# Optimization experiments

Measured on AMD Instinct MI355X. Metric: run time of the kernel, lower is better.

The kernel has to match this reference:

```python
import jax, jax.numpy as jnp
import numpy as np

HIDDEN = 1024
D_MEM = 256
BATCH = 4
SEQ = 1024
EPS = 1e-6


def elu_plus_one(x):
    # F.elu(x) + 1 == exp(x) for x<0, x+1 for x>=0 (positive feature map)
    return jnp.where(x > 0, x + 1.0, jnp.exp(x))


def setup_inputs() -> dict:
    key = jax.random.key(0)
    ks = jax.random.split(key, 8)
    hidden_states = jax.random.normal(ks[0], (BATCH, SEQ, HIDDEN), dtype=jnp.float32)
    s = 1.0 / np.sqrt(HIDDEN)
    w_q = jax.random.normal(ks[1], (D_MEM, HIDDEN), dtype=jnp.float32) * s
    w_k = jax.random.normal(ks[2], (D_MEM, HIDDEN), dtype=jnp.float32) * s
    w_v = jax.random.normal(ks[3], (D_MEM, HIDDEN), dtype=jnp.float32) * s
    w_o = jax.random.normal(ks[4], (HIDDEN, D_MEM), dtype=jnp.float32) * (1.0 / np.sqrt(D_MEM))
    gate = jnp.zeros((1,), dtype=jnp.float32)
    # nonzero persistent memory state so retrieval path is exercised
    memory = jax.random.normal(ks[5], (D_MEM, D_MEM), dtype=jnp.float32) * 0.1
    memory_norm = jax.random.uniform(ks[6], (D_MEM,), dtype=jnp.float32) * 10.0 + 1.0
    return {
        "hidden_states": hidden_states,
        "w_q": w_q, "w_k": w_k, "w_v": w_v, "w_o": w_o,
        "gate": gate, "memory": memory, "memory_norm": memory_norm,
    }


def _retrieve(sigma_x, memory, memory_norm):
    # [b,s,d] @ [d,d] -> [b,s,d], normalized by sigma_x @ memory_norm
    a_unnorm = jnp.matmul(sigma_x, memory)
    norm = jnp.clip(jnp.matmul(sigma_x, memory_norm), EPS, None)[..., None]
    out = a_unnorm / norm
    # torch: if memory_norm.sum() < 1e-6 -> zeros
    return jnp.where(memory_norm.sum() < EPS, jnp.zeros_like(out), out)


def reference(hidden_states, w_q, w_k, w_v, w_o, gate, memory, memory_norm):
    b, s, _ = hidden_states.shape
    q = jnp.einsum('bsh,dh->bsd', hidden_states, w_q)
    k = jnp.einsum('bsh,dh->bsd', hidden_states, w_k)
    v = jnp.einsum('bsh,dh->bsd', hidden_states, w_v)

    sigma_q = elu_plus_one(q)
    sigma_k = elu_plus_one(k)

    # --- retrieval from compressive memory ---
    memory_output = _retrieve(sigma_q, memory, memory_norm)

    # --- causal linear attention within segment (cumsum form, as in source) ---
    kv = jnp.einsum('bsd,bse->bsde', sigma_k, v)          # [b,s,d,d]
    kv_cumsum = jnp.cumsum(kv, axis=1)                     # [b,s,d,d]
    k_cumsum = jnp.cumsum(sigma_k, axis=1)                 # [b,s,d]
    numerator = jnp.einsum('bsd,bsde->bse', sigma_q, kv_cumsum)
    denominator = jnp.clip(jnp.einsum('bsd,bsd->bs', sigma_q, k_cumsum), EPS, None)[..., None]
    local_output = numerator / denominator

    g = jax.nn.sigmoid(gate[0])
    combined = g * memory_output + (1.0 - g) * local_output
    output = jnp.einsum('bsd,hd->bsh', combined, w_o)

    # --- delta-rule memory update (detached in torch) ---
    retrieved_unnorm = jnp.matmul(sigma_k, memory)
    norm = jnp.clip(jnp.matmul(sigma_k, memory_norm), EPS, None)[..., None]
    delta_v = v - retrieved_unnorm / norm
    memory_update = jnp.einsum('bsd,bse->de', sigma_k, delta_v) / (b * s)
    new_memory = jax.lax.stop_gradient(memory + memory_update)
    z_update = sigma_k.sum(axis=(0, 1)) / b
    new_memory_norm = jax.lax.stop_gradient(memory_norm + z_update)

    return output, new_memory, new_memory_norm
```

## Files before the change

### kernel.cpp

```cpp
#include <hip/hip_runtime.h>


#define HIDDEN 1024
#define DMEM 256
#define BATCH 4
#define SEQ 1024
#define MTOT (BATCH * SEQ)
#define CHUNK 128
#define NCH (SEQ / CHUNK)
#define NCHT (BATCH * NCH)
#define EPSF 1e-6f

typedef __bf16 bf16x8 __attribute__((ext_vector_type(8)));
typedef __bf16 bf16x4 __attribute__((ext_vector_type(4)));
typedef float f32x4 __attribute__((ext_vector_type(4)));

#define GL_LDS(g, l)                                                                   \
  __builtin_amdgcn_global_load_lds((const __attribute__((address_space(1))) void*)(g), \
                                   (__attribute__((address_space(3))) void*)(l), 16, 0, 0)

__device__ __forceinline__ float elu1(float x) { return x > 0.f ? x + 1.f : __expf(x); }

__device__ __forceinline__ void stage128(const __bf16* p, long ld, int k0, __bf16* sm,
                                         int wave) {
  GL_LDS(p + k0, sm + wave * 512);
  GL_LDS(p + (size_t)64 * ld + k0, sm + 2048 + wave * 512);
  GL_LDS(p + k0 + 32, sm + 4096 + wave * 512);
  GL_LDS(p + (size_t)64 * ld + k0 + 32, sm + 4096 + 2048 + wave * 512);
}
__device__ __forceinline__ void stage64(const __bf16* p, int k0, __bf16* sm, int wave) {
  GL_LDS(p + k0, sm + wave * 512);
  GL_LDS(p + k0 + 32, sm + 2048 + wave * 512);
}

__device__ __forceinline__ void gemm128_bk64(const __bf16* aptr, long lda, const __bf16* bptr,
                                             long ldb, int klen, __bf16* smA, __bf16* smB,
                                             int wave, int wr, int wc, int quad, int l16,
                                             f32x4 (&acc)[4][4]) {
  for (int k0 = 0; k0 < klen; k0 += 64) {
    stage128(aptr, lda, k0, smA, wave);
    stage128(bptr, ldb, k0, smB, wave);
    __syncthreads();
#pragma unroll
    for (int h = 0; h < 2; ++h) {
      bf16x8 aF[4], bF[4];
#pragma unroll
      for (int i = 0; i < 4; ++i)
        aF[i] = *reinterpret_cast<const bf16x8*>(smA + h * 4096 +
                                                 (wr * 64 + i * 16 + l16) * 32 + quad * 8);
#pragma unroll
      for (int j = 0; j < 4; ++j)
        bF[j] = *reinterpret_cast<const bf16x8*>(smB + h * 4096 +
                                                 (wc * 64 + j * 16 + l16) * 32 + quad * 8);
#pragma unroll
      for (int i = 0; i < 4; ++i)
#pragma unroll
        for (int j = 0; j < 4; ++j)
          acc[i][j] = __builtin_amdgcn_mfma_f32_16x16x32_bf16(aF[i], bF[j], acc[i][j], 0, 0, 0);
    }
    __syncthreads();
  }
}

__device__ __forceinline__ void gemm64_bk64(const __bf16* aptr, const __bf16* bptr, long ldb,
                                            int klen, __bf16* smA, __bf16* smB, int wave,
                                            int wr, int wc, int quad, int l16,
                                            f32x4 (&acc)[2][4]) {
  for (int k0 = 0; k0 < klen; k0 += 64) {
    stage64(aptr, k0, smA, wave);
    stage128(bptr, ldb, k0, smB, wave);
    __syncthreads();
#pragma unroll
    for (int h = 0; h < 2; ++h) {
      bf16x8 aF[2], bF[4];
#pragma unroll
      for (int i = 0; i < 2; ++i)
        aF[i] = *reinterpret_cast<const bf16x8*>(smA + h * 2048 +
                                                 (wr * 32 + i * 16 + l16) * 32 + quad * 8);
#pragma unroll
      for (int j = 0; j < 4; ++j)
        bF[j] = *reinterpret_cast<const bf16x8*>(smB + h * 4096 +
                                                 (wc * 64 + j * 16 + l16) * 32 + quad * 8);
#pragma unroll
      for (int i = 0; i < 2; ++i)
#pragma unroll
        for (int j = 0; j < 4; ++j)
          acc[i][j] = __builtin_amdgcn_mfma_f32_16x16x32_bf16(aF[i], bF[j], acc[i][j], 0, 0, 0);
    }
    __syncthreads();
  }
}

__global__ void kprep(const float* __restrict__ hs, const float* __restrict__ wq,
                      const float* __restrict__ wk, const float* __restrict__ wv,
                      const float* __restrict__ wo, const float* __restrict__ mem,
                      __bf16* __restrict__ hsb, __bf16* __restrict__ wqkvb,
                      __bf16* __restrict__ wob, __bf16* __restrict__ memT,
                      float* __restrict__ out) {
  __shared__ float s[64][65];
  int b = blockIdx.x, tid = threadIdx.x;
  if (b < 4096) {
    int i = b * 256 + tid;
    float4 f = reinterpret_cast<const float4*>(hs)[i];
    bf16x4 h = {(__bf16)f.x, (__bf16)f.y, (__bf16)f.z, (__bf16)f.w};
    reinterpret_cast<bf16x4*>(hsb)[i] = h;
  } else if (b < 5120) {
    int y = (b - 4096) >> 8;
    const float* src = (y == 0) ? wq : (y == 1) ? wk : (y == 2) ? wv : wo;
    __bf16* dst = (y < 3) ? wqkvb + (size_t)y * (DMEM * HIDDEN) : wob;
    int i = ((b - 4096) & 255) * 256 + tid;
    float4 f = reinterpret_cast<const float4*>(src)[i];
    bf16x4 h = {(__bf16)f.x, (__bf16)f.y, (__bf16)f.z, (__bf16)f.w};
    reinterpret_cast<bf16x4*>(dst)[i] = h;
  } else if (b < 5136) {
    int t = b - 5120;
    int bx = t & 3, by = t >> 2;
    int r0 = tid >> 6, col = tid & 63;
#pragma unroll
    for (int it = 0; it < 16; ++it) {
      int row = it * 4 + r0;
      s[row][col] = mem[(size_t)(by * 64 + row) * DMEM + bx * 64 + col];
    }
    __syncthreads();
#pragma unroll
    for (int it = 0; it < 16; ++it) {
      int row = it * 4 + r0;
      memT[(size_t)(bx * 64 + row) * DMEM + by * 64 + col] = (__bf16)s[col][row];
    }
  } else {
    int g = (b - 5136) * 256 + tid;
    reinterpret_cast<float4*>(out + (size_t)MTOT * HIDDEN)[g] =
        reinterpret_cast<const float4*>(mem)[g];
  }
}

__global__ __launch_bounds__(256) void k1_qkv_mfma(
    const __bf16* __restrict__ X, const __bf16* __restrict__ W, __bf16* __restrict__ sqb,
    __bf16* __restrict__ skb, __bf16* __restrict__ skT, __bf16* __restrict__ vT) {
  __shared__ __bf16 As[4096];
  __shared__ __bf16 Bs[8192];
  int tid = threadIdx.x;
  int lane = tid & 63, wave = tid >> 6;
  int m0 = blockIdx.x * 64;
  int by = blockIdx.y;
  int wsel = by >> 1, n0 = (by & 1) * 128;
  const __bf16* aptr = X + (size_t)(m0 + (tid >> 2)) * HIDDEN + ((tid & 3) << 3);
  const __bf16* bptr = W + (size_t)(by * 128 + (tid >> 2)) * HIDDEN + ((tid & 3) << 3);
  int wr = wave >> 1, wc = wave & 1, quad = lane >> 4, l16 = lane & 15;
  f32x4 acc[2][4] = {};
  gemm64_bk64(aptr, bptr, HIDDEN, HIDDEN, As, Bs, wave, wr, wc, quad, l16, acc);
#pragma unroll
  for (int i = 0; i < 2; ++i)
#pragma unroll
    for (int j = 0; j < 4; ++j) {
      int mb = m0 + wr * 32 + i * 16 + quad * 4;
      int n = n0 + wc * 64 + j * 16 + l16;
      if (wsel == 0) {
#pragma unroll
        for (int r = 0; r < 4; ++r) sqb[(size_t)(mb + r) * DMEM + n] = (__bf16)elu1(acc[i][j][r]);
      } else if (wsel == 1) {
        bf16x4 t;
#pragma unroll
        for (int r = 0; r < 4; ++r) {
          float v = elu1(acc[i][j][r]);
          skb[(size_t)(mb + r) * DMEM + n] = (__bf16)v;
          t[r] = (__bf16)v;
        }
        *reinterpret_cast<bf16x4*>(skT + (size_t)n * MTOT + mb) = t;
      } else {
        bf16x4 t;
#pragma unroll
        for (int r = 0; r < 4; ++r) t[r] = (__bf16)acc[i][j][r];
        *reinterpret_cast<bf16x4*>(vT + (size_t)n * MTOT + mb) = t;
      }
    }
}

__global__ __launch_bounds__(256) void kC(const __bf16* __restrict__ vT,
                                          const __bf16* __restrict__ skT,
                                          const __bf16* __restrict__ sqb,
                                          const __bf16* __restrict__ skb,
                                          __bf16* __restrict__ kvcT, __bf16* __restrict__ scb,
                                          float* __restrict__ ksc) {
  __shared__ __bf16 As[4096];
  __shared__ __bf16 Bs[8192];
  int tid = threadIdx.x;
  int c = blockIdx.x;
  int y = blockIdx.y;
  if (y == 10) {
    int d = tid;
    float s = 0.f;
    for (int i = 0; i < CHUNK; ++i) s += (float)skb[(size_t)(c * CHUNK + i) * DMEM + d];
    ksc[c * DMEM + d] = s;
    return;
  }
  int lane = tid & 63, wave = tid >> 6;
  int wr = wave >> 1, wc = wave & 1, quad = lane >> 4, l16 = lane & 15;
  if (y < 8) {
    int e0 = (y >> 1) * 64, d0 = (y & 1) * 128;
    const __bf16* aptr = vT + (size_t)(e0 + (tid >> 2)) * MTOT + c * CHUNK + ((tid & 3) << 3);
    const __bf16* bptr = skT + (size_t)(d0 + (tid >> 2)) * MTOT + c * CHUNK + ((tid & 3) << 3);
    f32x4 acc[2][4] = {};
    gemm64_bk64(aptr, bptr, MTOT, CHUNK, As, Bs, wave, wr, wc, quad, l16, acc);
#pragma unroll
    for (int i = 0; i < 2; ++i)
#pragma unroll
      for (int j = 0; j < 4; ++j)
#pragma unroll
        for (int r = 0; r < 4; ++r) {
          int e = e0 + wr * 32 + i * 16 + quad * 4 + r;
          int d = d0 + wc * 64 + j * 16 + l16;
          kvcT[(size_t)c * DMEM * DMEM + (size_t)e * DMEM + d] = (__bf16)acc[i][j][r];
        }
  } else {
    int i0 = (y - 8) * 64;
    const __bf16* aptr = sqb + (size_t)(c * CHUNK + i0 + (tid >> 2)) * DMEM + ((tid & 3) << 3);
    const __bf16* bptr = skb + (size_t)(c * CHUNK + (tid >> 2)) * DMEM + ((tid & 3) << 3);
    f32x4 acc[2][4] = {};
    gemm64_bk64(aptr, bptr, DMEM, DMEM, As, Bs, wave, wr, wc, quad, l16, acc);
#pragma unroll
    for (int i = 0; i < 2; ++i)
#pragma unroll
      for (int j = 0; j < 4; ++j)
#pragma unroll
        for (int r = 0; r < 4; ++r) {
          int ii = i0 + wr * 32 + i * 16 + quad * 4 + r;
          int jj = wc * 64 + j * 16 + l16;
          scb[(size_t)c * CHUNK * CHUNK + (size_t)ii * CHUNK + jj] =
              (jj <= ii) ? (__bf16)acc[i][j][r] : (__bf16)0.f;
        }
  }
}

__global__ __launch_bounds__(256) void kD(const __bf16* __restrict__ kvcT,
                                          __bf16* __restrict__ kvpT,
                                          const float* __restrict__ ksc,
                                          const __bf16* __restrict__ scb,
                                          const __bf16* __restrict__ sqb,
                                          const __bf16* __restrict__ skb,
                                          const float* __restrict__ mnorm,
                                          float* __restrict__ den, float* __restrict__ qn,
                                          float* __restrict__ kn) {
  int vt = blockIdx.x;
  int tid = threadIdx.x;
  if (vt < 128) {
    int batch = vt >> 5;
    size_t idx8 = (size_t)(((vt & 31) * 256 + tid)) * 8;
    bf16x8 t[NCH];
#pragma unroll
    for (int c = 0; c < NCH; ++c)
      t[c] = *reinterpret_cast<const bf16x8*>(kvcT +
                                              (size_t)(batch * NCH + c) * DMEM * DMEM + idx8);
    float run[8] = {};
#pragma unroll
    for (int c = 0; c < NCH; ++c) {
      bf16x8 o;
#pragma unroll
      for (int r = 0; r < 8; ++r) o[r] = (__bf16)run[r];
      *reinterpret_cast<bf16x8*>(kvpT + (size_t)(batch * NCH + c) * DMEM * DMEM + idx8) = o;
#pragma unroll
      for (int r = 0; r < 8; ++r) run[r] += (float)t[c][r];
    }
  } else {
    int wave = tid >> 6, lane = tid & 63;
    int m = (vt - 128) * 4 + wave;
    int c = m >> 7;
    int i = m & 127;
    int cb = c & ~7;
    int cnt = c - cb;
    float s_sc = 0.f, s_d2 = 0.f, s_qn = 0.f, s_kn = 0.f;
    for (int j = lane; j < CHUNK; j += 64)
      s_sc += (float)scb[(size_t)c * CHUNK * CHUNK + (size_t)i * CHUNK + j];
    for (int d = lane; d < DMEM; d += 64) {
      float q = (float)sqb[(size_t)m * DMEM + d];
      float k = (float)skb[(size_t)m * DMEM + d];
      float kp = 0.f;
#pragma unroll
      for (int cc = 0; cc < 7; ++cc) {
        float v = ksc[(cb + cc) * DMEM + d];
        kp += (cc < cnt) ? v : 0.f;
      }
      s_d2 += q * kp;
      s_qn += q * mnorm[d];
      s_kn += k * mnorm[d];
    }
#pragma unroll
    for (int off = 32; off > 0; off >>= 1) {
      s_sc += __shfl_down(s_sc, off);
      s_d2 += __shfl_down(s_d2, off);
      s_qn += __shfl_down(s_qn, off);
      s_kn += __shfl_down(s_kn, off);
    }
    if (lane == 0) {
      den[m] = s_sc + s_d2;
      qn[m] = s_qn;
      kn[m] = s_kn;
    }
  }
}

__global__ __launch_bounds__(256) void kE(const __bf16* __restrict__ scb,
                                          const __bf16* __restrict__ sqb,
                                          const __bf16* __restrict__ skb,
                                          const __bf16* __restrict__ vT,
                                          const __bf16* __restrict__ kvpT,
                                          const __bf16* __restrict__ memT,
                                          const float* __restrict__ den,
                                          const float* __restrict__ qn,
                                          const float* __restrict__ kn,
                                          const float* __restrict__ gate,
                                          const float* __restrict__ mnorm,
                                          __bf16* __restrict__ combb, __bf16* __restrict__ dvT) {
  __shared__ __bf16 As[4096];
  __shared__ __bf16 B1s[8192];
  __shared__ __bf16 B2s[8192];
  __shared__ float warr[4];
  int tid = threadIdx.x;
  int lane = tid & 63, wave = tid >> 6;
  int wr = wave >> 1, wc = wave & 1, quad = lane >> 4, l16 = lane & 15;
  int bid = blockIdx.x;
  if (bid < 128) {
    float mv = mnorm[tid];
#pragma unroll
    for (int off = 32; off > 0; off >>= 1) mv += __shfl_down(mv, off);
    if (lane == 0) warr[wave] = mv;
    __syncthreads();
    float fl = ((warr[0] + warr[1] + warr[2] + warr[3]) < EPSF) ? 0.f : 1.f;
    __syncthreads();
    int c = bid >> 2, yy = bid & 3;
    int i0 = (yy >> 1) * 64, e0 = (yy & 1) * 128;
    f32x4 acc_loc[2][4] = {};
    f32x4 acc_mem[2][4] = {};
    {
      const __bf16* aptr =
          scb + (size_t)c * CHUNK * CHUNK + (size_t)(i0 + (tid >> 2)) * CHUNK + ((tid & 3) << 3);
      const __bf16* bptr = vT + (size_t)(e0 + (tid >> 2)) * MTOT + c * CHUNK + ((tid & 3) << 3);
      gemm64_bk64(aptr, bptr, MTOT, CHUNK, As, B1s, wave, wr, wc, quad, l16, acc_loc);
    }
    {
      const __bf16* aptr = sqb + (size_t)(c * CHUNK + i0 + (tid >> 2)) * DMEM + ((tid & 3) << 3);
      const __bf16* b1ptr =
          kvpT + (size_t)c * DMEM * DMEM + (size_t)(e0 + (tid >> 2)) * DMEM + ((tid & 3) << 3);
      const __bf16* b2ptr = memT + (size_t)(e0 + (tid >> 2)) * DMEM + ((tid & 3) << 3);
      for (int k0 = 0; k0 < DMEM; k0 += 64) {
        stage64(aptr, k0, As, wave);
        stage128(b1ptr, DMEM, k0, B1s, wave);
        stage128(b2ptr, DMEM, k0, B2s, wave);
        __syncthreads();
#pragma unroll
        for (int h = 0; h < 2; ++h) {
          bf16x8 aF[2], b1F[4], b2F[4];
#pragma unroll
          for (int i = 0; i < 2; ++i)
            aF[i] = *reinterpret_cast<const bf16x8*>(As + h * 2048 +
                                                     (wr * 32 + i * 16 + l16) * 32 + quad * 8);
#pragma unroll
          for (int j = 0; j < 4; ++j) {
            b1F[j] = *reinterpret_cast<const bf16x8*>(B1s + h * 4096 +
                                                      (wc * 64 + j * 16 + l16) * 32 + quad * 8);
            b2F[j] = *reinterpret_cast<const bf16x8*>(B2s + h * 4096 +
                                                      (wc * 64 + j * 16 + l16) * 32 + quad * 8);
          }
#pragma unroll
          for (int i = 0; i < 2; ++i)
#pragma unroll
            for (int j = 0; j < 4; ++j) {
              acc_loc[i][j] =
                  __builtin_amdgcn_mfma_f32_16x16x32_bf16(aF[i], b1F[j], acc_loc[i][j], 0, 0, 0);
              acc_mem[i][j] =
                  __builtin_amdgcn_mfma_f32_16x16x32_bf16(aF[i], b2F[j], acc_mem[i][j], 0, 0, 0);
            }
        }
        __syncthreads();
      }
    }
    float g = 1.f / (1.f + __expf(-gate[0]));
#pragma unroll
    for (int i = 0; i < 2; ++i) {
      int mb = c * CHUNK + i0 + wr * 32 + i * 16 + quad * 4;
      float dn[4], qv[4];
#pragma unroll
      for (int r = 0; r < 4; ++r) {
        dn[r] = fmaxf(den[mb + r], EPSF);
        qv[r] = fmaxf(qn[mb + r], EPSF);
      }
#pragma unroll
      for (int j = 0; j < 4; ++j) {
        int e = e0 + wc * 64 + j * 16 + l16;
#pragma unroll
        for (int r = 0; r < 4; ++r) {
          float comb = g * fl * acc_mem[i][j][r] / qv[r] + (1.f - g) * acc_loc[i][j][r] / dn[r];
          combb[(size_t)(mb + r) * DMEM + e] = (__bf16)comb;
        }
      }
    }
  } else {
    int t = bid - 128;
    int m0 = (t >> 1) * 64, n0 = (t & 1) * 128;
    const __bf16* aptr = skb + (size_t)(m0 + (tid >> 2)) * DMEM + ((tid & 3) << 3);
    const __bf16* bptr = memT + (size_t)(n0 + (tid >> 2)) * DMEM + ((tid & 3) << 3);
    f32x4 acc[2][4] = {};
    gemm64_bk64(aptr, bptr, DMEM, DMEM, As, B1s, wave, wr, wc, quad, l16, acc);
#pragma unroll
    for (int i = 0; i < 2; ++i) {
      int mb = m0 + wr * 32 + i * 16 + quad * 4;
      float kv[4];
#pragma unroll
      for (int r = 0; r < 4; ++r) kv[r] = fmaxf(kn[mb + r], EPSF);
#pragma unroll
      for (int j = 0; j < 4; ++j) {
        int n = n0 + wc * 64 + j * 16 + l16;
        bf16x4 vv = *reinterpret_cast<const bf16x4*>(vT + (size_t)n * MTOT + mb);
        bf16x4 tt;
#pragma unroll
        for (int r = 0; r < 4; ++r) tt[r] = (__bf16)((float)vv[r] - acc[i][j][r] / kv[r]);
        *reinterpret_cast<bf16x4*>(dvT + (size_t)n * MTOT + mb) = tt;
      }
    }
  }
}

__global__ __launch_bounds__(256) void kF(const __bf16* __restrict__ combb,
                                          const __bf16* __restrict__ wob,
                                          const __bf16* __restrict__ skT,
                                          const __bf16* __restrict__ dvT,
                                          const float* __restrict__ ksc,
                                          const float* __restrict__ mnorm,
                                          float* __restrict__ out) {
  __shared__ __bf16 As[8192];
  __shared__ __bf16 Bs[8192];
  int tid = threadIdx.x;
  int bid = blockIdx.x;
  if (bid == 384) {
    int d = tid;
    float s = 0.f;
    for (int c = 0; c < NCHT; ++c) s += ksc[c * DMEM + d];
    out[(size_t)MTOT * HIDDEN + DMEM * DMEM + d] = mnorm[d] + s * (1.f / (float)BATCH);
    return;
  }
  int lane = tid & 63, wave = tid >> 6;
  int wr = wave >> 1, wc = wave & 1, quad = lane >> 4, l16 = lane & 15;
  if (bid < 256) {
    int m0 = (bid & 31) * 128, by = bid >> 5;
    const __bf16* aptr = combb + (size_t)(m0 + (tid >> 2)) * DMEM + ((tid & 3) << 3);
    const __bf16* bptr = wob + (size_t)(by * 128 + (tid >> 2)) * DMEM + ((tid & 3) << 3);
    f32x4 acc[4][4] = {};
    gemm128_bk64(aptr, DMEM, bptr, DMEM, DMEM, As, Bs, wave, wr, wc, quad, l16, acc);
#pragma unroll
    for (int i = 0; i < 4; ++i)
#pragma unroll
      for (int j = 0; j < 4; ++j)
#pragma unroll
        for (int r = 0; r < 4; ++r) {
          int m = m0 + wr * 64 + i * 16 + quad * 4 + r;
          int n = by * 128 + wc * 64 + j * 16 + l16;
          out[(size_t)m * HIDDEN + n] = acc[i][j][r];
        }
  } else {
    int t = bid - 256;
    int kbase = (t >> 3) * 256;
    int yy = t & 7;
    int d0 = (yy >> 1) * 64, e0 = (yy & 1) * 128;
    const __bf16* aptr = skT + (size_t)(d0 + (tid >> 2)) * MTOT + kbase + ((tid & 3) << 3);
    const __bf16* bptr = dvT + (size_t)(e0 + (tid >> 2)) * MTOT + kbase + ((tid & 3) << 3);
    f32x4 acc[2][4] = {};
    gemm64_bk64(aptr, bptr, MTOT, 256, As, Bs, wave, wr, wc, quad, l16, acc);
    float* base = out + (size_t)MTOT * HIDDEN;
#pragma unroll
    for (int i = 0; i < 2; ++i)
#pragma unroll
      for (int j = 0; j < 4; ++j)
#pragma unroll
        for (int r = 0; r < 4; ++r) {
          int d = d0 + wr * 32 + i * 16 + quad * 4 + r;
          int e = e0 + wc * 64 + j * 16 + l16;
          atomicAdd(&base[(size_t)d * DMEM + e], acc[i][j][r] * (1.f / (float)MTOT));
        }
  }
}

extern "C" void kernel_launch(void* const* d_in, const int* in_sizes, int n_in,
                              void* d_out, int out_size, void* d_ws, size_t ws_size,
                              hipStream_t stream) {
  const float* hs = (const float*)d_in[0];
  const float* wq = (const float*)d_in[1];
  const float* wk = (const float*)d_in[2];
  const float* wv = (const float*)d_in[3];
  const float* wo = (const float*)d_in[4];
  const float* gate = (const float*)d_in[5];
  const float* mem = (const float*)d_in[6];
  const float* mnorm = (const float*)d_in[7];
  float* out = (float*)d_out;
  float* ws = (float*)d_ws;

  float* ksc = ws;
  float* den = ksc + 8192;
  float* qn = den + 4096;
  float* kn = qn + 4096;
  __bf16* kvcT = (__bf16*)(ws + 20480);
  __bf16* hsb = kvcT + (size_t)NCHT * DMEM * DMEM;
  __bf16* wqkvb = hsb + (size_t)MTOT * HIDDEN;
  __bf16* wob = wqkvb + (size_t)3 * DMEM * HIDDEN;
  __bf16* memT = wob + (size_t)HIDDEN * DMEM;
  __bf16* sqb = memT + (size_t)DMEM * DMEM;
  __bf16* skb = sqb + (size_t)MTOT * DMEM;
  __bf16* skT = skb + (size_t)MTOT * DMEM;
  __bf16* vT = skT + (size_t)MTOT * DMEM;
  __bf16* scb = vT + (size_t)MTOT * DMEM;
  __bf16* kvpT = scb + (size_t)NCHT * CHUNK * CHUNK;
  __bf16* combb = kvpT + (size_t)NCHT * DMEM * DMEM;
  __bf16* dvT = combb + (size_t)MTOT * DMEM;

  kprep<<<dim3(5200), 256, 0, stream>>>(hs, wq, wk, wv, wo, mem, hsb, wqkvb, wob, memT, out);
  k1_qkv_mfma<<<dim3(64, 6), 256, 0, stream>>>(hsb, wqkvb, sqb, skb, skT, vT);
  kC<<<dim3(NCHT, 11), 256, 0, stream>>>(vT, skT, sqb, skb, kvcT, scb, ksc);
  kD<<<dim3(1152), 256, 0, stream>>>(kvcT, kvpT, ksc, scb, sqb, skb, mnorm, den, qn, kn);
  kE<<<dim3(256), 256, 0, stream>>>(scb, sqb, skb, vT, kvpT, memT, den, qn, kn, gate, mnorm,
                                    combb, dvT);
  kF<<<dim3(385), 256, 0, stream>>>(combb, wob, skT, dvT, ksc, mnorm, out);
}
```

Measured before the change: 135.0 us.

## Rebalance grids: smaller QKV/out tiles, move delta-v computation into kC

The QKV projection kernel moves from 64x128 to 64x64 tiles, doubling its grid to 768 blocks. The out-projection in kF moves from 128x128 to 64x128 tiles, giving 512 blocks. The delta-v computation (sigma_k @ memory, normalised, subtracted from v) moves from kE into extra blocks of kC, which now computes its own k-norm dot product, so kE runs only the combine path. The aim is more parallelism on a GPU with many CUs and less load imbalance in kE, in exchange for less data reuse per tile.

```diff
diff --git a/kernel.cpp b/kernel.cpp
--- a/kernel.cpp
+++ b/kernel.cpp
@@ -33,35 +33,6 @@
   GL_LDS(p + k0 + 32, sm + 2048 + wave * 512);
 }
 
-__device__ __forceinline__ void gemm128_bk64(const __bf16* aptr, long lda, const __bf16* bptr,
-                                             long ldb, int klen, __bf16* smA, __bf16* smB,
-                                             int wave, int wr, int wc, int quad, int l16,
-                                             f32x4 (&acc)[4][4]) {
-  for (int k0 = 0; k0 < klen; k0 += 64) {
-    stage128(aptr, lda, k0, smA, wave);
-    stage128(bptr, ldb, k0, smB, wave);
-    __syncthreads();
-#pragma unroll
-    for (int h = 0; h < 2; ++h) {
-      bf16x8 aF[4], bF[4];
-#pragma unroll
-      for (int i = 0; i < 4; ++i)
-        aF[i] = *reinterpret_cast<const bf16x8*>(smA + h * 4096 +
-                                                 (wr * 64 + i * 16 + l16) * 32 + quad * 8);
-#pragma unroll
-      for (int j = 0; j < 4; ++j)
-        bF[j] = *reinterpret_cast<const bf16x8*>(smB + h * 4096 +
-                                                 (wc * 64 + j * 16 + l16) * 32 + quad * 8);
-#pragma unroll
-      for (int i = 0; i < 4; ++i)
-#pragma unroll
-        for (int j = 0; j < 4; ++j)
-          acc[i][j] = __builtin_amdgcn_mfma_f32_16x16x32_bf16(aF[i], bF[j], acc[i][j], 0, 0, 0);
-    }
-    __syncthreads();
-  }
-}
-
 __device__ __forceinline__ void gemm64_bk64(const __bf16* aptr, const __bf16* bptr, long ldb,
                                             int klen, __bf16* smA, __bf16* smB, int wave,
                                             int wr, int wc, int quad, int l16,
@@ -85,6 +56,35 @@
       for (int i = 0; i < 2; ++i)
 #pragma unroll
         for (int j = 0; j < 4; ++j)
+          acc[i][j] = __builtin_amdgcn_mfma_f32_16x16x32_bf16(aF[i], bF[j], acc[i][j], 0, 0, 0);
+    }
+    __syncthreads();
+  }
+}
+
+__device__ __forceinline__ void gemm64x64_bk64(const __bf16* aptr, const __bf16* bptr,
+                                               int klen, __bf16* smA, __bf16* smB, int wave,
+                                               int wr, int wc, int quad, int l16,
+                                               f32x4 (&acc)[2][2]) {
+  for (int k0 = 0; k0 < klen; k0 += 64) {
+    stage64(aptr, k0, smA, wave);
+    stage64(bptr, k0, smB, wave);
+    __syncthreads();
+#pragma unroll
+    for (int h = 0; h < 2; ++h) {
+      bf16x8 aF[2], bF[2];
+#pragma unroll
+      for (int i = 0; i < 2; ++i)
+        aF[i] = *reinterpret_cast<const bf16x8*>(smA + h * 2048 +
+                                                 (wr * 32 + i * 16 + l16) * 32 + quad * 8);
+#pragma unroll
+      for (int j = 0; j < 2; ++j)
+        bF[j] = *reinterpret_cast<const bf16x8*>(smB + h * 2048 +
+                                                 (wc * 32 + j * 16 + l16) * 32 + quad * 8);
+#pragma unroll
+      for (int i = 0; i < 2; ++i)
+#pragma unroll
+        for (int j = 0; j < 2; ++j)
           acc[i][j] = __builtin_amdgcn_mfma_f32_16x16x32_bf16(aF[i], bF[j], acc[i][j], 0, 0, 0);
     }
     __syncthreads();
@@ -138,23 +138,24 @@
     const __bf16* __restrict__ X, const __bf16* __restrict__ W, __bf16* __restrict__ sqb,
     __bf16* __restrict__ skb, __bf16* __restrict__ skT, __bf16* __restrict__ vT) {
   __shared__ __bf16 As[4096];
-  __shared__ __bf16 Bs[8192];
+  __shared__ __bf16 Bs[4096];
   int tid = threadIdx.x;
   int lane = tid & 63, wave = tid >> 6;
   int m0 = blockIdx.x * 64;
   int by = blockIdx.y;
-  int wsel = by >> 1, n0 = (by & 1) * 128;
+  int wsel = by >> 2, n0 = (by & 3) * 64;
   const __bf16* aptr = X + (size_t)(m0 + (tid >> 2)) * HIDDEN + ((tid & 3) << 3);
-  const __bf16* bptr = W + (size_t)(by * 128 + (tid >> 2)) * HIDDEN + ((tid & 3) << 3);
+  const __bf16* bptr =
+      W + (size_t)(wsel * DMEM + n0 + (tid >> 2)) * HIDDEN + ((tid & 3) << 3);
   int wr = wave >> 1, wc = wave & 1, quad = lane >> 4, l16 = lane & 15;
-  f32x4 acc[2][4] = {};
-  gemm64_bk64(aptr, bptr, HIDDEN, HIDDEN, As, Bs, wave, wr, wc, quad, l16, acc);
+  f32x4 acc[2][2] = {};
+  gemm64x64_bk64(aptr, bptr, HIDDEN, As, Bs, wave, wr, wc, quad, l16, acc);
 #pragma unroll
   for (int i = 0; i < 2; ++i)
 #pragma unroll
-    for (int j = 0; j < 4; ++j) {
+    for (int j = 0; j < 2; ++j) {
       int mb = m0 + wr * 32 + i * 16 + quad * 4;
-      int n = n0 + wc * 64 + j * 16 + l16;
+      int n = n0 + wc * 32 + j * 16 + l16;
       if (wsel == 0) {
 #pragma unroll
         for (int r = 0; r < 4; ++r) sqb[(size_t)(mb + r) * DMEM + n] = (__bf16)elu1(acc[i][j][r]);
@@ -176,14 +177,17 @@
     }
 }
 
-__global__ __launch_bounds__(256) void kC(const __bf16* __restrict__ vT,
-                                          const __bf16* __restrict__ skT,
-                                          const __bf16* __restrict__ sqb,
-                                          const __bf16* __restrict__ skb,
-                                          __bf16* __restrict__ kvcT, __bf16* __restrict__ scb,
-                                          float* __restrict__ ksc) {
+__global__ __launch_bounds__(256) void kC2(const __bf16* __restrict__ vT,
+                                           const __bf16* __restrict__ skT,
+                                           const __bf16* __restrict__ sqb,
+                                           const __bf16* __restrict__ skb,
+                                           const __bf16* __restrict__ memT,
+                                           const float* __restrict__ mnorm,
+                                           __bf16* __restrict__ kvcT, __bf16* __restrict__ scb,
+                                           float* __restrict__ ksc, __bf16* __restrict__ dvT) {
   __shared__ __bf16 As[4096];
   __shared__ __bf16 Bs[8192];
+  __shared__ float knl[64];
   int tid = threadIdx.x;
   int c = blockIdx.x;
   int y = blockIdx.y;
@@ -212,7 +216,7 @@
           int d = d0 + wc * 64 + j * 16 + l16;
           kvcT[(size_t)c * DMEM * DMEM + (size_t)e * DMEM + d] = (__bf16)acc[i][j][r];
         }
-  } else {
+  } else if (y < 10) {
     int i0 = (y - 8) * 64;
     const __bf16* aptr = sqb + (size_t)(c * CHUNK + i0 + (tid >> 2)) * DMEM + ((tid & 3) << 3);
     const __bf16* bptr = skb + (size_t)(c * CHUNK + (tid >> 2)) * DMEM + ((tid & 3) << 3);
@@ -229,6 +233,38 @@
           scb[(size_t)c * CHUNK * CHUNK + (size_t)ii * CHUNK + jj] =
               (jj <= ii) ? (__bf16)acc[i][j][r] : (__bf16)0.f;
         }
+  } else {
+    int t = (y - 11) * 32 + c;
+    int m0 = (t >> 1) * 64, n0 = (t & 1) * 128;
+    for (int rr = 0; rr < 16; ++rr) {
+      int m = m0 + wave * 16 + rr;
+      float s = 0.f;
+      for (int d = lane; d < DMEM; d += 64) s += (float)skb[(size_t)m * DMEM + d] * mnorm[d];
+#pragma unroll
+      for (int off = 32; off > 0; off >>= 1) s += __shfl_down(s, off);
+      if (lane == 0) knl[wave * 16 + rr] = s;
+    }
+    __syncthreads();
+    const __bf16* aptr = skb + (size_t)(m0 + (tid >> 2)) * DMEM + ((tid & 3) << 3);
+    const __bf16* bptr = memT + (size_t)(n0 + (tid >> 2)) * DMEM + ((tid & 3) << 3);
+    f32x4 acc[2][4] = {};
+    gemm64_bk64(aptr, bptr, DMEM, DMEM, As, Bs, wave, wr, wc, quad, l16, acc);
+#pragma unroll
+    for (int i = 0; i < 2; ++i) {
+      int rel = wr * 32 + i * 16 + quad * 4;
+      float kv[4];
+#pragma unroll
+      for (int r = 0; r < 4; ++r) kv[r] = fmaxf(knl[rel + r], EPSF);
+#pragma unroll
+      for (int j = 0; j < 4; ++j) {
+        int n = n0 + wc * 64 + j * 16 + l16;
+        bf16x4 vv = *reinterpret_cast<const bf16x4*>(vT + (size_t)n * MTOT + m0 + rel);
+        bf16x4 tt;
+#pragma unroll
+        for (int r = 0; r < 4; ++r) tt[r] = (__bf16)((float)vv[r] - acc[i][j][r] / kv[r]);
+        *reinterpret_cast<bf16x4*>(dvT + (size_t)n * MTOT + m0 + rel) = tt;
+      }
+    }
   }
 }
 
@@ -237,10 +273,8 @@
                                           const float* __restrict__ ksc,
                                           const __bf16* __restrict__ scb,
                                           const __bf16* __restrict__ sqb,
-                                          const __bf16* __restrict__ skb,
                                           const float* __restrict__ mnorm,
-                                          float* __restrict__ den, float* __restrict__ qn,
-                                          float* __restrict__ kn) {
+                                          float* __restrict__ den, float* __restrict__ qn) {
   int vt = blockIdx.x;
   int tid = threadIdx.x;
   if (vt < 128) {
@@ -268,12 +302,11 @@
     int i = m & 127;
     int cb = c & ~7;
     int cnt = c - cb;
-    float s_sc = 0.f, s_d2 = 0.f, s_qn = 0.f, s_kn = 0.f;
+    float s_sc = 0.f, s_d2 = 0.f, s_qn = 0.f;
     for (int j = lane; j < CHUNK; j += 64)
       s_sc += (float)scb[(size_t)c * CHUNK * CHUNK + (size_t)i * CHUNK + j];
     for (int d = lane; d < DMEM; d += 64) {
       float q = (float)sqb[(size_t)m * DMEM + d];
-      float k = (float)skb[(size_t)m * DMEM + d];
       float kp = 0.f;
 #pragma unroll
       for (int cc = 0; cc < 7; ++cc) {
@@ -282,35 +315,30 @@
       }
       s_d2 += q * kp;
       s_qn += q * mnorm[d];
-      s_kn += k * mnorm[d];
     }
 #pragma unroll
     for (int off = 32; off > 0; off >>= 1) {
       s_sc += __shfl_down(s_sc, off);
       s_d2 += __shfl_down(s_d2, off);
       s_qn += __shfl_down(s_qn, off);
-      s_kn += __shfl_down(s_kn, off);
     }
     if (lane == 0) {
       den[m] = s_sc + s_d2;
       qn[m] = s_qn;
-      kn[m] = s_kn;
     }
   }
 }
 
 __global__ __launch_bounds__(256) void kE(const __bf16* __restrict__ scb,
                                           const __bf16* __restrict__ sqb,
-                                          const __bf16* __restrict__ skb,
                                           const __bf16* __restrict__ vT,
                                           const __bf16* __restrict__ kvpT,
                                           const __bf16* __restrict__ memT,
                                           const float* __restrict__ den,
                                           const float* __restrict__ qn,
-                                          const float* __restrict__ kn,
                                           const float* __restrict__ gate,
                                           const float* __restrict__ mnorm,
-                                          __bf16* __restrict__ combb, __bf16* __restrict__ dvT) {
+                                          __bf16* __restrict__ combb) {
   __shared__ __bf16 As[4096];
   __shared__ __bf16 B1s[8192];
   __shared__ __bf16 B2s[8192];
@@ -319,102 +347,77 @@
   int lane = tid & 63, wave = tid >> 6;
   int wr = wave >> 1, wc = wave & 1, quad = lane >> 4, l16 = lane & 15;
   int bid = blockIdx.x;
-  if (bid < 128) {
-    float mv = mnorm[tid];
-#pragma unroll
-    for (int off = 32; off > 0; off >>= 1) mv += __shfl_down(mv, off);
-    if (lane == 0) warr[wave] = mv;
-    __syncthreads();
-    float fl = ((warr[0] + warr[1] + warr[2] + warr[3]) < EPSF) ? 0.f : 1.f;
-    __syncthreads();
-    int c = bid >> 2, yy = bid & 3;
-    int i0 = (yy >> 1) * 64, e0 = (yy & 1) * 128;
-    f32x4 acc_loc[2][4] = {};
-    f32x4 acc_mem[2][4] = {};
-    {
-      const __bf16* aptr =
-          scb + (size_t)c * CHUNK * CHUNK + (size_t)(i0 + (tid >> 2)) * CHUNK + ((tid & 3) << 3);
-      const __bf16* bptr = vT + (size_t)(e0 + (tid >> 2)) * MTOT + c * CHUNK + ((tid & 3) << 3);
-      gemm64_bk64(aptr, bptr, MTOT, CHUNK, As, B1s, wave, wr, wc, quad, l16, acc_loc);
-    }
-    {
-      const __bf16* aptr = sqb + (size_t)(c * CHUNK + i0 + (tid >> 2)) * DMEM + ((tid & 3) << 3);
-      const __bf16* b1ptr =
-          kvpT + (size_t)c * DMEM * DMEM + (size_t)(e0 + (tid >> 2)) * DMEM + ((tid & 3) << 3);
-      const __bf16* b2ptr = memT + (size_t)(e0 + (tid >> 2)) * DMEM + ((tid & 3) << 3);
-      for (int k0 = 0; k0 < DMEM; k0 += 64) {
-        stage64(aptr, k0, As, wave);
-        stage128(b1ptr, DMEM, k0, B1s, wave);
-        stage128(b2ptr, DMEM, k0, B2s, wave);
-        __syncthreads();
-#pragma unroll
-        for (int h = 0; h < 2; ++h) {
-          bf16x8 aF[2], b1F[4], b2F[4];
-#pragma unroll
-          for (int i = 0; i < 2; ++i)
-            aF[i] = *reinterpret_cast<const bf16x8*>(As + h * 2048 +
-                                                     (wr * 32 + i * 16 + l16) * 32 + quad * 8);
+  float mv = mnorm[tid];
+#pragma unroll
+  for (int off = 32; off > 0; off >>= 1) mv += __shfl_down(mv, off);
+  if (lane == 0) warr[wave] = mv;
+  __syncthreads();
+  float fl = ((warr[0] + warr[1] + warr[2] + warr[3]) < EPSF) ? 0.f : 1.f;
+  __syncthreads();
+  int c = bid >> 2, yy = bid & 3;
+  int i0 = (yy >> 1) * 64, e0 = (yy & 1) * 128;
+  f32x4 acc_loc[2][4] = {};
+  f32x4 acc_mem[2][4] = {};
+  {
+    const __bf16* aptr =
+        scb + (size_t)c * CHUNK * CHUNK + (size_t)(i0 + (tid >> 2)) * CHUNK + ((tid & 3) << 3);
+    const __bf16* bptr = vT + (size_t)(e0 + (tid >> 2)) * MTOT + c * CHUNK + ((tid & 3) << 3);
+    gemm64_bk64(aptr, bptr, MTOT, CHUNK, As, B1s, wave, wr, wc, quad, l16, acc_loc);
+  }
+  {
+    const __bf16* aptr = sqb + (size_t)(c * CHUNK + i0 + (tid >> 2)) * DMEM + ((tid & 3) << 3);
+    const __bf16* b1ptr =
+        kvpT + (size_t)c * DMEM * DMEM + (size_t)(e0 + (tid >> 2)) * DMEM + ((tid & 3) << 3);
+    const __bf16* b2ptr = memT + (size_t)(e0 + (tid >> 2)) * DMEM + ((tid & 3) << 3);
+    for (int k0 = 0; k0 < DMEM; k0 += 64) {
+      stage64(aptr, k0, As, wave);
+      stage128(b1ptr, DMEM, k0, B1s, wave);
+      stage128(b2ptr, DMEM, k0, B2s, wave);
+      __syncthreads();
+#pragma unroll
+      for (int h = 0; h < 2; ++h) {
+        bf16x8 aF[2], b1F[4], b2F[4];
+#pragma unroll
+        for (int i = 0; i < 2; ++i)
+          aF[i] = *reinterpret_cast<const bf16x8*>(As + h * 2048 +
+                                                   (wr * 32 + i * 16 + l16) * 32 + quad * 8);
+#pragma unroll
+        for (int j = 0; j < 4; ++j) {
+          b1F[j] = *reinterpret_cast<const bf16x8*>(B1s + h * 4096 +
+                                                    (wc * 64 + j * 16 + l16) * 32 + quad * 8);
+          b2F[j] = *reinterpret_cast<const bf16x8*>(B2s + h * 4096 +
+                                                    (wc * 64 + j * 16 + l16) * 32 + quad * 8);
+        }
+#pragma unroll
+        for (int i = 0; i < 2; ++i)
 #pragma unroll
           for (int j = 0; j < 4; ++j) {
-            b1F[j] = *reinterpret_cast<const bf16x8*>(B1s + h * 4096 +
-                                                      (wc * 64 + j * 16 + l16) * 32 + quad * 8);
-            b2F[j] = *reinterpret_cast<const bf16x8*>(B2s + h * 4096 +
-                                                      (wc * 64 + j * 16 + l16) * 32 + quad * 8);
+            acc_loc[i][j] =
+                __builtin_amdgcn_mfma_f32_16x16x32_bf16(aF[i], b1F[j], acc_loc[i][j], 0, 0, 0);
+            acc_mem[i][j] =
+                __builtin_amdgcn_mfma_f32_16x16x32_bf16(aF[i], b2F[j], acc_mem[i][j], 0, 0, 0);
           }
-#pragma unroll
-          for (int i = 0; i < 2; ++i)
-#pragma unroll
-            for (int j = 0; j < 4; ++j) {
-              acc_loc[i][j] =
-                  __builtin_amdgcn_mfma_f32_16x16x32_bf16(aF[i], b1F[j], acc_loc[i][j], 0, 0, 0);
-              acc_mem[i][j] =
-                  __builtin_amdgcn_mfma_f32_16x16x32_bf16(aF[i], b2F[j], acc_mem[i][j], 0, 0, 0);
-            }
-        }
-        __syncthreads();
       }
-    }
-    float g = 1.f / (1.f + __expf(-gate[0]));
-#pragma unroll
-    for (int i = 0; i < 2; ++i) {
-      int mb = c * CHUNK + i0 + wr * 32 + i * 16 + quad * 4;
-      float dn[4], qv[4];
+      __syncthreads();
+    }
+  }
+  float g = 1.f / (1.f + __expf(-gate[0]));
+#pragma unroll
+  for (int i = 0; i < 2; ++i) {
+    int mb = c * CHUNK + i0 + wr * 32 + i * 16 + quad * 4;
+    float dn[4], qv[4];
+#pragma unroll
+    for (int r = 0; r < 4; ++r) {
+      dn[r] = fmaxf(den[mb + r], EPSF);
+      qv[r] = fmaxf(qn[mb + r], EPSF);
+    }
+#pragma unroll
+    for (int j = 0; j < 4; ++j) {
+      int e = e0 + wc * 64 + j * 16 + l16;
 #pragma unroll
       for (int r = 0; r < 4; ++r) {
-        dn[r] = fmaxf(den[mb + r], EPSF);
-        qv[r] = fmaxf(qn[mb + r], EPSF);
-      }
-#pragma unroll
-      for (int j = 0; j < 4; ++j) {
-        int e = e0 + wc * 64 + j * 16 + l16;
-#pragma unroll
-        for (int r = 0; r < 4; ++r) {
-          float comb = g * fl * acc_mem[i][j][r] / qv[r] + (1.f - g) * acc_loc[i][j][r] / dn[r];
-          combb[(size_t)(mb + r) * DMEM + e] = (__bf16)comb;
-        }
-      }
-    }
-  } else {
-    int t = bid - 128;
-    int m0 = (t >> 1) * 64, n0 = (t & 1) * 128;
-    const __bf16* aptr = skb + (size_t)(m0 + (tid >> 2)) * DMEM + ((tid & 3) << 3);
-    const __bf16* bptr = memT + (size_t)(n0 + (tid >> 2)) * DMEM + ((tid & 3) << 3);
-    f32x4 acc[2][4] = {};
-    gemm64_bk64(aptr, bptr, DMEM, DMEM, As, B1s, wave, wr, wc, quad, l16, acc);
-#pragma unroll
-    for (int i = 0; i < 2; ++i) {
-      int mb = m0 + wr * 32 + i * 16 + quad * 4;
-      float kv[4];
-#pragma unroll
-      for (int r = 0; r < 4; ++r) kv[r] = fmaxf(kn[mb + r], EPSF);
-#pragma unroll
-      for (int j = 0; j < 4; ++j) {
-        int n = n0 + wc * 64 + j * 16 + l16;
-        bf16x4 vv = *reinterpret_cast<const bf16x4*>(vT + (size_t)n * MTOT + mb);
-        bf16x4 tt;
-#pragma unroll
-        for (int r = 0; r < 4; ++r) tt[r] = (__bf16)((float)vv[r] - acc[i][j][r] / kv[r]);
-        *reinterpret_cast<bf16x4*>(dvT + (size_t)n * MTOT + mb) = tt;
+        float comb = g * fl * acc_mem[i][j][r] / qv[r] + (1.f - g) * acc_loc[i][j][r] / dn[r];
+        combb[(size_t)(mb + r) * DMEM + e] = (__bf16)comb;
       }
     }
   }
@@ -427,11 +430,11 @@
                                           const float* __restrict__ ksc,
                                           const float* __restrict__ mnorm,
                                           float* __restrict__ out) {
-  __shared__ __bf16 As[8192];
+  __shared__ __bf16 As[4096];
   __shared__ __bf16 Bs[8192];
   int tid = threadIdx.x;
   int bid = blockIdx.x;
-  if (bid == 384) {
+  if (bid == 640) {
     int d = tid;
     float s = 0.f;
     for (int c = 0; c < NCHT; ++c) s += ksc[c * DMEM + d];
@@ -440,24 +443,24 @@
   }
   int lane = tid & 63, wave = tid >> 6;
   int wr = wave >> 1, wc = wave & 1, quad = lane >> 4, l16 = lane & 15;
-  if (bid < 256) {
-    int m0 = (bid & 31) * 128, by = bid >> 5;
+  if (bid < 512) {
+    int m0 = (bid & 63) * 64, by = bid >> 6;
     const __bf16* aptr = combb + (size_t)(m0 + (tid >> 2)) * DMEM + ((tid & 3) << 3);
     const __bf16* bptr = wob + (size_t)(by * 128 + (tid >> 2)) * DMEM + ((tid & 3) << 3);
-    f32x4 acc[4][4] = {};
-    gemm128_bk64(aptr, DMEM, bptr, DMEM, DMEM, As, Bs, wave, wr, wc, quad, l16, acc);
-#pragma unroll
-    for (int i = 0; i < 4; ++i)
+    f32x4 acc[2][4] = {};
+    gemm64_bk64(aptr, bptr, DMEM, DMEM, As, Bs, wave, wr, wc, quad, l16, acc);
+#pragma unroll
+    for (int i = 0; i < 2; ++i)
 #pragma unroll
       for (int j = 0; j < 4; ++j)
 #pragma unroll
         for (int r = 0; r < 4; ++r) {
-          int m = m0 + wr * 64 + i * 16 + quad * 4 + r;
+          int m = m0 + wr * 32 + i * 16 + quad * 4 + r;
           int n = by * 128 + wc * 64 + j * 16 + l16;
           out[(size_t)m * HIDDEN + n] = acc[i][j][r];
         }
   } else {
-    int t = bid - 256;
+    int t = bid - 512;
     int kbase = (t >> 3) * 256;
     int yy = t & 7;
     int d0 = (yy >> 1) * 64, e0 = (yy & 1) * 128;
@@ -496,7 +499,6 @@
   float* ksc = ws;
   float* den = ksc + 8192;
   float* qn = den + 4096;
-  float* kn = qn + 4096;
   __bf16* kvcT = (__bf16*)(ws + 20480);
   __bf16* hsb = kvcT + (size_t)NCHT * DMEM * DMEM;
   __bf16* wqkvb = hsb + (size_t)MTOT * HIDDEN;
@@ -512,10 +514,9 @@
   __bf16* dvT = combb + (size_t)MTOT * DMEM;
 
   kprep<<<dim3(5200), 256, 0, stream>>>(hs, wq, wk, wv, wo, mem, hsb, wqkvb, wob, memT, out);
-  k1_qkv_mfma<<<dim3(64, 6), 256, 0, stream>>>(hsb, wqkvb, sqb, skb, skT, vT);
-  kC<<<dim3(NCHT, 11), 256, 0, stream>>>(vT, skT, sqb, skb, kvcT, scb, ksc);
-  kD<<<dim3(1152), 256, 0, stream>>>(kvcT, kvpT, ksc, scb, sqb, skb, mnorm, den, qn, kn);
-  kE<<<dim3(256), 256, 0, stream>>>(scb, sqb, skb, vT, kvpT, memT, den, qn, kn, gate, mnorm,
-                                    combb, dvT);
-  kF<<<dim3(385), 256, 0, stream>>>(combb, wob, skT, dvT, ksc, mnorm, out);
-}
+  k1_qkv_mfma<<<dim3(64, 12), 256, 0, stream>>>(hsb, wqkvb, sqb, skb, skT, vT);
+  kC2<<<dim3(NCHT, 15), 256, 0, stream>>>(vT, skT, sqb, skb, memT, mnorm, kvcT, scb, ksc, dvT);
+  kD<<<dim3(1152), 256, 0, stream>>>(kvcT, kvpT, ksc, scb, sqb, mnorm, den, qn);
+  kE<<<dim3(128), 256, 0, stream>>>(scb, sqb, vT, kvpT, memT, den, qn, gate, mnorm, combb);
+  kF<<<dim3(641), 256, 0, stream>>>(combb, wob, skT, dvT, ksc, mnorm, out);
+}
```

After: 153.0 us. 1.13x slower.
